# Optimization experiments

Measured on AMD Instinct MI355X. Metric: run time of the kernel, lower is better.

## Reference

```python
import jax, jax.numpy as jnp
import numpy as np

FEAT = 1433
HID = 2
NUM_CLASS = 7
EPS = 1e-5  # torch BatchNorm1d default eps


def _bn_softsign(h, gamma, beta):
    # BatchNorm1d in training mode: batch stats over (batch, length) per channel.
    mu = h.mean(axis=(0, 2), keepdims=True)
    var = h.var(axis=(0, 2), keepdims=True)  # biased, matches torch normalization
    hn = (h - mu) * jax.lax.rsqrt(var + EPS)
    hn = hn * gamma[None, :, None] + beta[None, :, None]
    return hn / (1.0 + jnp.abs(hn))  # Softsign


def feature_adjacency(x, y):
    # (x.unsqueeze(-1) * y.unsqueeze(-2)).sum(dim=1) with x channel dim == 1
    # reduces to an outer product of x[:,0] with neighbor.sum over K.
    adj = jnp.einsum('bf,bg->bfg', x.sum(1), y.sum(1))  # [B,F,F]
    adj = adj + jnp.swapaxes(adj, -1, -2)
    adj = jnp.sqrt(adj)
    # row_normalize: divide by sum over dim 1, zero out inf/nan
    norm = adj / adj.sum(axis=1, keepdims=True)
    norm = jnp.where(jnp.isfinite(norm), norm, 0.0)
    return norm + jnp.eye(FEAT, dtype=x.dtype)


def featbrd(x, adj, W, b):
    # adjacency-based feature conv: y[b,c,f] = sum_g adj[(b),f,g] x[b,c,g],
    # then 1x1 conv over channels (Conv1d kernel_size=1).
    if adj.shape[0] == 1:
        y = jnp.einsum('fg,bcg->bcf', adj[0], x)
    else:
        y = jnp.einsum('bfg,bcg->bcf', adj, x)
    return jnp.einsum('oc,bcf->bof', W, y) + b[None, :, None]


def setup_inputs() -> dict:
    key = jax.random.key(0)
    ks = jax.random.split(key, 10)
    B, K = 64, 8
    inp = {
        'x': jax.random.uniform(ks[0], (B, 1, FEAT), dtype=jnp.float32),
        'neighbor': jax.random.uniform(ks[1], (B, K, FEAT), dtype=jnp.float32),
        'adj_buf': jnp.zeros((1, FEAT, FEAT), jnp.float32),
        'W1': jax.random.normal(ks[2], (HID, 1), jnp.float32) * 0.5,
        'b1': jnp.zeros((HID,), jnp.float32),
        'W2': jax.random.normal(ks[3], (HID, HID), jnp.float32) * 0.5,
        'b2': jnp.zeros((HID,), jnp.float32),
        'g1': jnp.ones((HID,), jnp.float32),
        'be1': jnp.zeros((HID,), jnp.float32),
        'g2': jnp.ones((HID,), jnp.float32),
        'be2': jnp.zeros((HID,), jnp.float32),
        'Wc': jax.random.normal(ks[4], (NUM_CLASS, FEAT * HID), jnp.float32) * 0.02,
        'bc': jnp.zeros((NUM_CLASS,), jnp.float32),
    }
    return inp


def reference(x, neighbor, adj_buf, W1, b1, W2, b2, g1, be1, g2, be2, Wc, bc):
    fadj = feature_adjacency(x, neighbor)          # [B,F,F]
    adj_tot = adj_buf + fadj.sum(0)                # [1,F,F] (buffer starts at zero)
    h = _bn_softsign(featbrd(x, fadj, W1, b1), g1, be1)      # [B,HID,F]
    h = _bn_softsign(featbrd(h, adj_tot, W2, b2), g2, be2)   # [B,HID,F]
    flat = h.reshape(h.shape[0], -1)               # Flatten (C then F, row-major)
    return flat @ Wc.T + bc
```

## Files before the change

### kernel.cpp

```cpp
#include <hip/hip_runtime.h>
#include <hip/hip_bf16.h>
#include <math.h>

constexpr int F   = 1433;
constexpr int NB  = 64;
constexpr int KN  = 8;
constexpr int BF  = NB * F;
constexpr float EPS = 1e-5f;

constexpr int SF  = 16;
constexpr int CH  = 90;
constexpr int AbS = 1440;
constexpr int SK  = 15;
constexpr int FT  = 12;
constexpr int NA  = 720;
constexpr int NST = 256;

constexpr int O_YS  = 0;
constexpr int O_DP  = O_YS + BF;
constexpr int O_Y1P = O_DP + SF * BF;
constexpr int O_P   = O_Y1P + SF * BF;
constexpr int O_Y1  = O_P + 4 * BF;
constexpr int O_Y2  = O_Y1 + BF;
constexpr int O_G2P = O_Y2 + 2 * BF;
constexpr int O_AB  = O_G2P + SK * 128 * F;
constexpr int O_ST  = O_AB + (F * AbS) / 2;

__global__ __launch_bounds__(256) void k_D(const float* __restrict__ x,
                                           const float* __restrict__ nbr,
                                           float* __restrict__ DP,
                                           float* __restrict__ ys_out,
                                           float* __restrict__ st) {
  const int b = blockIdx.x, s = blockIdx.y;
  if (b == 0 && s == 0 && threadIdx.x < 64) st[threadIdx.x] = 0.f;
  __shared__ __align__(8) float2 xyc[CH];
  const int cs = s * CH, cn = min(CH, F - cs);
  for (int i = threadIdx.x; i < cn; i += 256) {
    const float* p = nbr + (size_t)b * KN * F + cs + i;
    float a = 0.f;
#pragma unroll
    for (int k = 0; k < KN; ++k) a += p[k * F];
    xyc[i] = make_float2(x[b * F + cs + i], a);
  }
  __syncthreads();
  float gx[6], gy[6], acc[6] = {};
#pragma unroll
  for (int j = 0; j < 6; ++j) {
    int g = threadIdx.x + 256 * j;
    int gc = min(g, F - 1);
    const float* p = nbr + (size_t)b * KN * F + gc;
    float a = 0.f;
#pragma unroll
    for (int k = 0; k < KN; ++k) a += p[k * F];
    gx[j] = (g < F) ? x[b * F + gc] : 0.f;
    gy[j] = (g < F) ? a : 0.f;
  }
  if (s == 0) {
#pragma unroll
    for (int j = 0; j < 6; ++j) {
      int g = threadIdx.x + 256 * j;
      if (g < F) ys_out[b * F + g] = gy[j];
    }
  }
#pragma unroll 6
  for (int i = 0; i < cn; ++i) {
    float2 p = xyc[i];
#pragma unroll
    for (int j = 0; j < 6; ++j)
      acc[j] += __builtin_amdgcn_sqrtf(fmaf(gy[j], p.x, gx[j] * p.y));
  }
#pragma unroll
  for (int j = 0; j < 6; ++j) {
    int g = threadIdx.x + 256 * j;
    if (g < F) DP[(size_t)s * BF + b * F + g] = acc[j];
  }
}

__global__ __launch_bounds__(256) void k_y1(const float* __restrict__ x,
                                            const float* __restrict__ ys,
                                            const float* __restrict__ DP,
                                            float* __restrict__ Y1P,
                                            float4* __restrict__ P) {
  __shared__ __align__(16) float4 pl[CH];
  const int b = blockIdx.x, s = blockIdx.y;
  const int cs = s * CH, cn = min(CH, F - cs);
  for (int i = threadIdx.x; i < cn; i += 256) {
    int g = cs + i;
    float d = 0.f;
#pragma unroll
    for (int t = 0; t < SF; ++t) d += DP[(size_t)t * BF + b * F + g];
    float inv = (d > 0.f) ? 1.f / d : 0.f;
    float xv = x[b * F + g], yv = ys[b * F + g];
    float4 pv = make_float4(xv, yv, xv * inv, inv);
    pl[i] = pv;
    P[b * F + g] = pv;
  }
  __syncthreads();
  float fx[6], fy[6], acc[6] = {};
#pragma unroll
  for (int j = 0; j < 6; ++j) {
    int f = threadIdx.x + 256 * j;
    fx[j] = (f < F) ? x[b * F + f] : 0.f;
    fy[j] = (f < F) ? ys[b * F + f] : 0.f;
  }
#pragma unroll 6
  for (int i = 0; i < cn; ++i) {
    float4 p = pl[i];
#pragma unroll
    for (int j = 0; j < 6; ++j)
      acc[j] = fmaf(__builtin_amdgcn_sqrtf(fmaf(fx[j], p.y, fy[j] * p.x)), p.z, acc[j]);
  }
#pragma unroll
  for (int j = 0; j < 6; ++j) {
    int f = threadIdx.x + 256 * j;
    if (f < F) Y1P[(size_t)s * BF + b * F + f] = acc[j];
  }
}

__global__ __launch_bounds__(256) void k_Astats(const float* __restrict__ x,
                                                const float* __restrict__ ys,
                                                const float4* __restrict__ P,
                                                const float* __restrict__ Y1P,
                                                __hip_bfloat16* __restrict__ Ab,
                                                float* __restrict__ y1,
                                                float* __restrict__ st) {
  const int bid = blockIdx.x;
  if (bid < NA) {
    __shared__ float2 fxy[FT][NB];
    const int gxc = bid % 6, fy = bid / 6;
    const int fbase = fy * FT;
#pragma unroll
    for (int r = 0; r < 3; ++r) {
      int i = threadIdx.x + 256 * r;
      int j = i >> 6, bb = i & 63;
      int f = fbase + j;
      float vx = 0.f, vy = 0.f;
      if (f < F) { vx = x[bb * F + f]; vy = ys[bb * F + f]; }
      fxy[j][bb] = make_float2(vx, vy);
    }
    __syncthreads();
    const int g = gxc * 256 + threadIdx.x;
    if (g >= AbS) return;
    if (g < F) {
      float acc[FT] = {};
      float4 cur[4], nxt[4];
#pragma unroll
      for (int t = 0; t < 4; ++t) cur[t] = P[t * F + g];
      for (int bb = 0; bb < NB; bb += 4) {
        if (bb + 4 < NB) {
#pragma unroll
          for (int t = 0; t < 4; ++t) nxt[t] = P[(bb + 4 + t) * F + g];
        }
#pragma unroll
        for (int t = 0; t < 4; ++t) {
          float4 pc = cur[t];
#pragma unroll
          for (int j = 0; j < FT; ++j) {
            float2 w = fxy[j][bb + t];
            acc[j] = fmaf(__builtin_amdgcn_sqrtf(fmaf(w.x, pc.y, pc.x * w.y)), pc.w, acc[j]);
          }
        }
#pragma unroll
        for (int t = 0; t < 4; ++t) cur[t] = nxt[t];
      }
#pragma unroll
      for (int j = 0; j < FT; ++j) {
        int f = fbase + j;
        if (f < F) Ab[(size_t)f * AbS + g] = __float2bfloat16(acc[j]);
      }
    } else {
#pragma unroll
      for (int j = 0; j < FT; ++j) {
        int f = fbase + j;
        if (f < F) Ab[(size_t)f * AbS + g] = __float2bfloat16(0.f);
      }
    }
  } else {
    const int sid = bid - NA;
    float sv = 0.f, sq = 0.f;
    for (int i = sid * 256 + threadIdx.x; i < BF; i += NST * 256) {
      float v = x[i];
#pragma unroll
      for (int t = 0; t < SF; ++t) v += Y1P[(size_t)t * BF + i];
      y1[i] = v;
      sv += v; sq += v * v;
    }
#pragma unroll
    for (int o = 32; o; o >>= 1) {
      sv += __shfl_down(sv, o, 64);
      sq += __shfl_down(sq, o, 64);
    }
    __shared__ float ls[4], lq[4];
    int wave = threadIdx.x >> 6, lane = threadIdx.x & 63;
    if (lane == 0) { ls[wave] = sv; lq[wave] = sq; }
    __syncthreads();
    if (threadIdx.x == 0) {
      atomicAdd(&st[0], ls[0] + ls[1] + ls[2] + ls[3]);
      atomicAdd(&st[1], lq[0] + lq[1] + lq[2] + lq[3]);
    }
  }
}

__global__ __launch_bounds__(256, 4) void k_gemm(const ushort* __restrict__ Ab,
                                                 const float* __restrict__ y1,
                                                 const float* __restrict__ st,
                                                 const float* __restrict__ W1,
                                                 const float* __restrict__ g1,
                                                 const float* __restrict__ be1,
                                                 float* __restrict__ G2P) {
  const float mu = st[0] / (float)BF;
  const float var = st[1] / (float)BF - mu * mu;
  const float wa = W1[0], wb = W1[1];
  const float k0 = wa * g1[0] / sqrtf(wa * wa * var + EPS);
  const float k1 = wb * g1[1] / sqrtf(wb * wb * var + EPS);
  const float c0 = -k0 * mu + be1[0];
  const float c1 = -k1 * mu + be1[1];

  __shared__ __align__(16) float Al[32 * 36];
  __shared__ __align__(16) float Hl[32 * 132];
  const int f0 = blockIdx.x * 32;
  const int gs = blockIdx.y * 96;
  const int tid = threadIdx.x;
  const int ffs = tid >> 3, g4s = (tid & 7) * 4;
  const int hb = tid & 7, hg = tid >> 3;
  const int fsub = (tid & 7) * 4, msub = (tid >> 3) * 4;

  uint2 pa; float pyv[8];
  auto loadRegs = [&](int gb) {
    const int f = f0 + ffs;
    pa = make_uint2(0u, 0u);
    if (f < F) pa = *(const uint2*)&Ab[(size_t)f * AbS + gb + g4s];
    const int gl = min(gb + hg, F - 1);
#pragma unroll
    for (int r = 0; r < 8; ++r) pyv[r] = y1[(hb + 8 * r) * F + gl];
  };
  auto storeLDS = [&]() {
    Al[(g4s + 0) * 36 + ffs] = __uint_as_float(pa.x << 16);
    Al[(g4s + 1) * 36 + ffs] = __uint_as_float(pa.x & 0xffff0000u);
    Al[(g4s + 2) * 36 + ffs] = __uint_as_float(pa.y << 16);
    Al[(g4s + 3) * 36 + ffs] = __uint_as_float(pa.y & 0xffff0000u);
#pragma unroll
    for (int r = 0; r < 8; ++r) {
      const int bb = hb + 8 * r;
      const float v = pyv[r];
      float h0 = fmaf(k0, v, c0); h0 = h0 / (1.f + fabsf(h0));
      float h1 = fmaf(k1, v, c1); h1 = h1 / (1.f + fabsf(h1));
      *(float2*)&Hl[hg * 132 + 2 * bb] = make_float2(h0, h1);
    }
  };

  float acc[4][4] = {};
  loadRegs(gs);
  for (int c = 0; c < 3; ++c) {
    if (c) __syncthreads();
    storeLDS();
    __syncthreads();
    if (c < 2) loadRegs(gs + (c + 1) * 32);
#pragma unroll 4
    for (int gi = 0; gi < 32; ++gi) {
      float4 a4 = *(const float4*)&Al[gi * 36 + fsub];
      float4 h4 = *(const float4*)&Hl[gi * 132 + msub];
      float av[4] = {a4.x, a4.y, a4.z, a4.w};
      float hv[4] = {h4.x, h4.y, h4.z, h4.w};
#pragma unroll
      for (int i = 0; i < 4; ++i)
#pragma unroll
        for (int j = 0; j < 4; ++j)
          acc[i][j] = fmaf(av[i], hv[j], acc[i][j]);
    }
  }
  float* dst = G2P + (size_t)blockIdx.y * 128 * F;
#pragma unroll
  for (int i = 0; i < 4; ++i) {
    int f = f0 + fsub + i;
    if (f < F) {
#pragma unroll
      for (int j = 0; j < 4; ++j)
        dst[(msub + j) * F + f] = acc[i][j];
    }
  }
}

__global__ __launch_bounds__(256) void k_stats2(const float* __restrict__ y1,
                                                const float* __restrict__ G2P,
                                                const float* __restrict__ st,
                                                const float* __restrict__ W1,
                                                const float* __restrict__ g1,
                                                const float* __restrict__ be1,
                                                float* __restrict__ y2,
                                                float* __restrict__ stw) {
  const float mu = st[0] / (float)BF;
  const float var = st[1] / (float)BF - mu * mu;
  const float wa = W1[0], wb = W1[1];
  const float k0 = wa * g1[0] / sqrtf(wa * wa * var + EPS);
  const float k1 = wb * g1[1] / sqrtf(wb * wb * var + EPS);
  const float c0 = -k0 * mu + be1[0];
  const float c1 = -k1 * mu + be1[1];

  float su = 0.f, sv = 0.f, suu = 0.f, svv = 0.f, suv = 0.f;
  for (int i = blockIdx.x * 256 + threadIdx.x; i < BF; i += gridDim.x * 256) {
    int b = i / F, f = i - b * F;
    float w = y1[i];
    float h0 = fmaf(k0, w, c0); h0 = h0 / (1.f + fabsf(h0));
    float h1 = fmaf(k1, w, c1); h1 = h1 / (1.f + fabsf(h1));
    int iu = (2 * b) * F + f, iv = iu + F;
    float u = 64.f * h0, v = 64.f * h1;
#pragma unroll
    for (int t = 0; t < SK; ++t) {
      u += G2P[(size_t)t * 128 * F + iu];
      v += G2P[(size_t)t * 128 * F + iv];
    }
    y2[iu] = u; y2[iv] = v;
    su += u; sv += v; suu += u * u; svv += v * v; suv += u * v;
  }
#pragma unroll
  for (int o = 32; o; o >>= 1) {
    su += __shfl_down(su, o, 64);
    sv += __shfl_down(sv, o, 64);
    suu += __shfl_down(suu, o, 64);
    svv += __shfl_down(svv, o, 64);
    suv += __shfl_down(suv, o, 64);
  }
  __shared__ float red[5][4];
  int wave = threadIdx.x >> 6, lane = threadIdx.x & 63;
  if (lane == 0) {
    red[0][wave] = su; red[1][wave] = sv; red[2][wave] = suu;
    red[3][wave] = svv; red[4][wave] = suv;
  }
  __syncthreads();
  if (threadIdx.x == 0) {
#pragma unroll
    for (int m = 0; m < 5; ++m)
      atomicAdd(&stw[2 + m], red[m][0] + red[m][1] + red[m][2] + red[m][3]);
  }
}

__global__ __launch_bounds__(256) void k_out(const float* __restrict__ y2,
                                             const float* __restrict__ st,
                                             const float* __restrict__ W2,
                                             const float* __restrict__ b2,
                                             const float* __restrict__ g2,
                                             const float* __restrict__ be2,
                                             const float* __restrict__ Wc,
                                             const float* __restrict__ bc,
                                             float* __restrict__ out) {
  float n = (float)BF;
  float Eu = st[2] / n, Ev = st[3] / n;
  float Euu = st[4] / n, Evv = st[5] / n, Euv = st[6] / n;
  float cA[2], cB[2], cC[2];
#pragma unroll
  for (int o = 0; o < 2; ++o) {
    float w0 = W2[o * 2 + 0], w1 = W2[o * 2 + 1];
    float mean = w0 * Eu + w1 * Ev + b2[o];
    float Eh2 = w0 * w0 * Euu + 2.f * w0 * w1 * Euv + w1 * w1 * Evv +
                2.f * b2[o] * (w0 * Eu + w1 * Ev) + b2[o] * b2[o];
    float vr = Eh2 - mean * mean;
    float inv = g2[o] / sqrtf(vr + EPS);
    cA[o] = w0 * inv;
    cB[o] = w1 * inv;
    cC[o] = (b2[o] - mean) * inv + be2[o];
  }
  const int b = blockIdx.x;
  float acc[7] = {};
  for (int f = threadIdx.x; f < F; f += 256) {
    float u = y2[(2 * b) * F + f], v = y2[(2 * b + 1) * F + f];
    float h0 = fmaf(cA[0], u, fmaf(cB[0], v, cC[0]));
    h0 = h0 / (1.f + fabsf(h0));
    float h1 = fmaf(cA[1], u, fmaf(cB[1], v, cC[1]));
    h1 = h1 / (1.f + fabsf(h1));
#pragma unroll
    for (int o = 0; o < 7; ++o) acc[o] = fmaf(Wc[o * (2 * F) + f], h0, acc[o]);
#pragma unroll
    for (int o = 0; o < 7; ++o) acc[o] = fmaf(Wc[o * (2 * F) + F + f], h1, acc[o]);
  }
#pragma unroll
  for (int o = 0; o < 7; ++o) {
#pragma unroll
    for (int s = 32; s; s >>= 1) acc[o] += __shfl_down(acc[o], s, 64);
  }
  __shared__ float red[7][4];
  int wave = threadIdx.x >> 6, lane = threadIdx.x & 63;
  if (lane == 0) {
#pragma unroll
    for (int o = 0; o < 7; ++o) red[o][wave] = acc[o];
  }
  __syncthreads();
  if (threadIdx.x < 7) {
    int o = threadIdx.x;
    out[b * 7 + o] = red[o][0] + red[o][1] + red[o][2] + red[o][3] + bc[o];
  }
}

extern "C" void kernel_launch(void* const* d_in, const int* in_sizes, int n_in,
                              void* d_out, int out_size, void* d_ws, size_t ws_size,
                              hipStream_t stream) {
  const float* x    = (const float*)d_in[0];
  const float* nbr  = (const float*)d_in[1];
  const float* W1   = (const float*)d_in[3];
  const float* W2   = (const float*)d_in[5];
  const float* b2   = (const float*)d_in[6];
  const float* g1   = (const float*)d_in[7];
  const float* be1  = (const float*)d_in[8];
  const float* g2   = (const float*)d_in[9];
  const float* be2  = (const float*)d_in[10];
  const float* Wc   = (const float*)d_in[11];
  const float* bc   = (const float*)d_in[12];
  float* out = (float*)d_out;
  float* ws  = (float*)d_ws;

  float*  ys  = ws + O_YS;
  float*  DP  = ws + O_DP;
  float*  Y1P = ws + O_Y1P;
  float4* P   = (float4*)(ws + O_P);
  float*  y1  = ws + O_Y1;
  float*  y2  = ws + O_Y2;
  float*  G2P = ws + O_G2P;
  __hip_bfloat16* Ab = (__hip_bfloat16*)(ws + O_AB);
  float*  st  = ws + O_ST;

  k_D     <<<dim3(NB, SF), 256, 0, stream>>>(x, nbr, DP, ys, st);
  k_y1    <<<dim3(NB, SF), 256, 0, stream>>>(x, ys, DP, Y1P, P);
  k_Astats<<<NA + NST, 256, 0, stream>>>(x, ys, P, Y1P, Ab, y1, st);
  k_gemm  <<<dim3(45, SK), 256, 0, stream>>>((const ushort*)Ab, y1, st, W1, g1, be1, G2P);
  k_stats2<<<NST, 256, 0, stream>>>(y1, G2P, st, W1, g1, be1, y2, st);
  k_out   <<<NB, 256, 0, stream>>>(y2, st, W2, b2, g2, be2, Wc, bc, out);
}
```

Measured before the change: 205.1 us.

## Fuse six-kernel pipeline into one persistent kernel with grid barriers

New measurement: 571.9 us. 2.79x slower.

```diff
diff --git a/kernel.cpp b/kernel.cpp
--- a/kernel.cpp
+++ b/kernel.cpp
@@ -25,6 +25,400 @@
 constexpr int O_G2P = O_Y2 + 2 * BF;
 constexpr int O_AB  = O_G2P + SK * 128 * F;
 constexpr int O_ST  = O_AB + (F * AbS) / 2;
+constexpr int O_BAR = O_ST + 64;
+
+__device__ __forceinline__ void grid_barrier(unsigned* cnt, unsigned* flag,
+                                             unsigned phase) {
+  __syncthreads();
+  if (threadIdx.x == 0) {
+    __threadfence();
+    unsigned t = atomicAdd(cnt, 1u);
+    if (t == phase * gridDim.x - 1u) {
+      __hip_atomic_store(flag, phase, __ATOMIC_RELEASE, __HIP_MEMORY_SCOPE_AGENT);
+    } else {
+      while (__hip_atomic_load(flag, __ATOMIC_ACQUIRE, __HIP_MEMORY_SCOPE_AGENT) < phase)
+        __builtin_amdgcn_s_sleep(2);
+    }
+    __threadfence();
+  }
+  __syncthreads();
+}
+
+__global__ __launch_bounds__(256, 4) void k_fused(
+    const float* __restrict__ x, const float* __restrict__ nbr,
+    const float* __restrict__ W1, const float* __restrict__ g1,
+    const float* __restrict__ be1, const float* __restrict__ W2,
+    const float* __restrict__ b2, const float* __restrict__ g2,
+    const float* __restrict__ be2, const float* __restrict__ Wc,
+    const float* __restrict__ bc, float* __restrict__ out,
+    float* __restrict__ ws) {
+  float*  ys  = ws + O_YS;
+  float*  DP  = ws + O_DP;
+  float*  Y1P = ws + O_Y1P;
+  float4* P   = (float4*)(ws + O_P);
+  float*  y1  = ws + O_Y1;
+  float*  y2  = ws + O_Y2;
+  float*  G2P = ws + O_G2P;
+  __hip_bfloat16* Ab = (__hip_bfloat16*)(ws + O_AB);
+  const ushort*   Abu = (const ushort*)(ws + O_AB);
+  float*  st  = ws + O_ST;
+  unsigned* bcnt  = (unsigned*)(ws + O_BAR);
+  unsigned* bflag = bcnt + 1;
+
+  __shared__ __align__(16) char smem[21504];
+  const int tid = threadIdx.x;
+  const int gsz = (int)gridDim.x;
+
+  {
+    float2* xyc = (float2*)smem;
+    for (int w = blockIdx.x; w < NB * SF; w += gsz) {
+      const int b = w & 63, s = w >> 6;
+      if (w == 0 && tid < 64) st[tid] = 0.f;
+      if (w == 1 && tid < NB * 7) out[tid] = bc[tid % 7];
+      __syncthreads();
+      const int cs = s * CH, cn = min(CH, F - cs);
+      for (int i = tid; i < cn; i += 256) {
+        const float* p = nbr + (size_t)b * KN * F + cs + i;
+        float a = 0.f;
+#pragma unroll
+        for (int k = 0; k < KN; ++k) a += p[k * F];
+        xyc[i] = make_float2(x[b * F + cs + i], a);
+      }
+      __syncthreads();
+      float gx[6], gy[6], acc[6] = {};
+#pragma unroll
+      for (int j = 0; j < 6; ++j) {
+        int g = tid + 256 * j;
+        int gc = min(g, F - 1);
+        const float* p = nbr + (size_t)b * KN * F + gc;
+        float a = 0.f;
+#pragma unroll
+        for (int k = 0; k < KN; ++k) a += p[k * F];
+        gx[j] = (g < F) ? x[b * F + gc] : 0.f;
+        gy[j] = (g < F) ? a : 0.f;
+      }
+      if (s == 0) {
+#pragma unroll
+        for (int j = 0; j < 6; ++j) {
+          int g = tid + 256 * j;
+          if (g < F) ys[b * F + g] = gy[j];
+        }
+      }
+#pragma unroll 6
+      for (int i = 0; i < cn; ++i) {
+        float2 p = xyc[i];
+#pragma unroll
+        for (int j = 0; j < 6; ++j)
+          acc[j] += __builtin_amdgcn_sqrtf(fmaf(gy[j], p.x, gx[j] * p.y));
+      }
+#pragma unroll
+      for (int j = 0; j < 6; ++j) {
+        int g = tid + 256 * j;
+        if (g < F) DP[(size_t)s * BF + b * F + g] = acc[j];
+      }
+    }
+  }
+  grid_barrier(bcnt, bflag, 1u);
+
+  {
+    float4* pl = (float4*)smem;
+    for (int w = blockIdx.x; w < NB * SF; w += gsz) {
+      const int b = w & 63, s = w >> 6;
+      __syncthreads();
+      const int cs = s * CH, cn = min(CH, F - cs);
+      for (int i = tid; i < cn; i += 256) {
+        int g = cs + i;
+        float d = 0.f;
+#pragma unroll
+        for (int t = 0; t < SF; ++t) d += DP[(size_t)t * BF + b * F + g];
+        float inv = (d > 0.f) ? 1.f / d : 0.f;
+        float xv = x[b * F + g], yv = ys[b * F + g];
+        float4 pv = make_float4(xv, yv, xv * inv, inv);
+        pl[i] = pv;
+        P[b * F + g] = pv;
+      }
+      __syncthreads();
+      float fx[6], fys[6], acc[6] = {};
+#pragma unroll
+      for (int j = 0; j < 6; ++j) {
+        int f = tid + 256 * j;
+        fx[j]  = (f < F) ? x[b * F + f] : 0.f;
+        fys[j] = (f < F) ? ys[b * F + f] : 0.f;
+      }
+#pragma unroll 6
+      for (int i = 0; i < cn; ++i) {
+        float4 p = pl[i];
+#pragma unroll
+        for (int j = 0; j < 6; ++j)
+          acc[j] = fmaf(__builtin_amdgcn_sqrtf(fmaf(fx[j], p.y, fys[j] * p.x)), p.z, acc[j]);
+      }
+#pragma unroll
+      for (int j = 0; j < 6; ++j) {
+        int f = tid + 256 * j;
+        if (f < F) Y1P[(size_t)s * BF + b * F + f] = acc[j];
+      }
+    }
+  }
+  grid_barrier(bcnt, bflag, 2u);
+
+  {
+    for (int w = blockIdx.x; w < NA + NST; w += gsz) {
+      __syncthreads();
+      if (w < NA) {
+        float2 (*fxy)[NB] = (float2(*)[NB])smem;
+        const int gxc = w % 6, fyt = w / 6;
+        const int fbase = fyt * FT;
+#pragma unroll
+        for (int r = 0; r < 3; ++r) {
+          int i = tid + 256 * r;
+          int j = i >> 6, bb = i & 63;
+          int f = fbase + j;
+          float vx = 0.f, vy = 0.f;
+          if (f < F) { vx = x[bb * F + f]; vy = ys[bb * F + f]; }
+          fxy[j][bb] = make_float2(vx, vy);
+        }
+        __syncthreads();
+        const int g = gxc * 256 + tid;
+        if (g < F) {
+          float acc[FT] = {};
+          float4 cur[4], nxt[4];
+#pragma unroll
+          for (int t = 0; t < 4; ++t) cur[t] = P[t * F + g];
+          for (int bb = 0; bb < NB; bb += 4) {
+            if (bb + 4 < NB) {
+#pragma unroll
+              for (int t = 0; t < 4; ++t) nxt[t] = P[(bb + 4 + t) * F + g];
+            }
+#pragma unroll
+            for (int t = 0; t < 4; ++t) {
+              float4 pc = cur[t];
+#pragma unroll
+              for (int j = 0; j < FT; ++j) {
+                float2 wv = fxy[j][bb + t];
+                acc[j] = fmaf(__builtin_amdgcn_sqrtf(fmaf(wv.x, pc.y, pc.x * wv.y)), pc.w, acc[j]);
+              }
+            }
+#pragma unroll
+            for (int t = 0; t < 4; ++t) cur[t] = nxt[t];
+          }
+#pragma unroll
+          for (int j = 0; j < FT; ++j) {
+            int f = fbase + j;
+            if (f < F) Ab[(size_t)f * AbS + g] = __float2bfloat16(acc[j]);
+          }
+        } else if (g < AbS) {
+#pragma unroll
+          for (int j = 0; j < FT; ++j) {
+            int f = fbase + j;
+            if (f < F) Ab[(size_t)f * AbS + g] = __float2bfloat16(0.f);
+          }
+        }
+      } else {
+        const int sid = w - NA;
+        float sv = 0.f, sq = 0.f;
+        for (int i = sid * 256 + tid; i < BF; i += NST * 256) {
+          float v = x[i];
+#pragma unroll
+          for (int t = 0; t < SF; ++t) v += Y1P[(size_t)t * BF + i];
+          y1[i] = v;
+          sv += v; sq += v * v;
+        }
+#pragma unroll
+        for (int o = 32; o; o >>= 1) {
+          sv += __shfl_down(sv, o, 64);
+          sq += __shfl_down(sq, o, 64);
+        }
+        float* ls = (float*)smem;
+        float* lq = ls + 4;
+        int wave = tid >> 6, lane = tid & 63;
+        if (lane == 0) { ls[wave] = sv; lq[wave] = sq; }
+        __syncthreads();
+        if (tid == 0) {
+          atomicAdd(&st[0], ls[0] + ls[1] + ls[2] + ls[3]);
+          atomicAdd(&st[1], lq[0] + lq[1] + lq[2] + lq[3]);
+        }
+      }
+    }
+  }
+  grid_barrier(bcnt, bflag, 3u);
+
+  {
+    const float mu  = st[0] / (float)BF;
+    const float var = st[1] / (float)BF - mu * mu;
+    const float wa = W1[0], wb = W1[1];
+    const float k0 = wa * g1[0] / sqrtf(wa * wa * var + EPS);
+    const float k1 = wb * g1[1] / sqrtf(wb * wb * var + EPS);
+    const float c0 = -k0 * mu + be1[0];
+    const float c1 = -k1 * mu + be1[1];
+
+    float* Al = (float*)smem;
+    float* Hl = (float*)(smem + 4608);
+    const int ffs = tid >> 3, g4s = (tid & 7) * 4;
+    const int hb = tid & 7, hg = tid >> 3;
+    const int fsub = (tid & 7) * 4, msub = (tid >> 3) * 4;
+
+    for (int w = blockIdx.x; w < 45 * SK; w += gsz) {
+      const int fb = w % 45, sk = w / 45;
+      const int f0 = fb * 32;
+      const int gs = sk * 96;
+      __syncthreads();
+
+      uint2 pa; float pyv[8];
+      auto loadRegs = [&](int gb) {
+        const int f = f0 + ffs;
+        pa = make_uint2(0u, 0u);
+        if (f < F) pa = *(const uint2*)&Abu[(size_t)f * AbS + gb + g4s];
+        const int gl = min(gb + hg, F - 1);
+#pragma unroll
+        for (int r = 0; r < 8; ++r) pyv[r] = y1[(hb + 8 * r) * F + gl];
+      };
+      auto storeLDS = [&]() {
+        Al[(g4s + 0) * 36 + ffs] = __uint_as_float(pa.x << 16);
+        Al[(g4s + 1) * 36 + ffs] = __uint_as_float(pa.x & 0xffff0000u);
+        Al[(g4s + 2) * 36 + ffs] = __uint_as_float(pa.y << 16);
+        Al[(g4s + 3) * 36 + ffs] = __uint_as_float(pa.y & 0xffff0000u);
+#pragma unroll
+        for (int r = 0; r < 8; ++r) {
+          const int bb = hb + 8 * r;
+          const float v = pyv[r];
+          float h0 = fmaf(k0, v, c0); h0 = h0 / (1.f + fabsf(h0));
+          float h1 = fmaf(k1, v, c1); h1 = h1 / (1.f + fabsf(h1));
+          *(float2*)&Hl[hg * 132 + 2 * bb] = make_float2(h0, h1);
+        }
+      };
+
+      float acc[4][4] = {};
+      loadRegs(gs);
+      for (int c = 0; c < 3; ++c) {
+        if (c) __syncthreads();
+        storeLDS();
+        __syncthreads();
+        if (c < 2) loadRegs(gs + (c + 1) * 32);
+#pragma unroll 4
+        for (int gi = 0; gi < 32; ++gi) {
+          float4 a4 = *(const float4*)&Al[gi * 36 + fsub];
+          float4 h4 = *(const float4*)&Hl[gi * 132 + msub];
+          float av[4] = {a4.x, a4.y, a4.z, a4.w};
+          float hv[4] = {h4.x, h4.y, h4.z, h4.w};
+#pragma unroll
+          for (int i = 0; i < 4; ++i)
+#pragma unroll
+            for (int j = 0; j < 4; ++j)
+              acc[i][j] = fmaf(av[i], hv[j], acc[i][j]);
+        }
+      }
+      float* dst = G2P + (size_t)sk * 128 * F;
+#pragma unroll
+      for (int i = 0; i < 4; ++i) {
+        int f = f0 + fsub + i;
+        if (f < F) {
+#pragma unroll
+          for (int j = 0; j < 4; ++j)
+            dst[(msub + j) * F + f] = acc[i][j];
+        }
+      }
+    }
+  }
+  grid_barrier(bcnt, bflag, 4u);
+
+  {
+    const float mu  = st[0] / (float)BF;
+    const float var = st[1] / (float)BF - mu * mu;
+    const float wa = W1[0], wb = W1[1];
+    const float k0 = wa * g1[0] / sqrtf(wa * wa * var + EPS);
+    const float k1 = wb * g1[1] / sqrtf(wb * wb * var + EPS);
+    const float c0 = -k0 * mu + be1[0];
+    const float c1 = -k1 * mu + be1[1];
+
+    float su = 0.f, sv = 0.f, suu = 0.f, svv = 0.f, suv = 0.f;
+    for (int i = blockIdx.x * 256 + tid; i < BF; i += gsz * 256) {
+      int b = i / F, f = i - b * F;
+      float wv = y1[i];
+      float h0 = fmaf(k0, wv, c0); h0 = h0 / (1.f + fabsf(h0));
+      float h1 = fmaf(k1, wv, c1); h1 = h1 / (1.f + fabsf(h1));
+      int iu = (2 * b) * F + f, iv = iu + F;
+      float u = 64.f * h0, v = 64.f * h1;
+#pragma unroll
+      for (int t = 0; t < SK; ++t) {
+        u += G2P[(size_t)t * 128 * F + iu];
+        v += G2P[(size_t)t * 128 * F + iv];
+      }
+      y2[iu] = u; y2[iv] = v;
+      su += u; sv += v; suu += u * u; svv += v * v; suv += u * v;
+    }
+#pragma unroll
+    for (int o = 32; o; o >>= 1) {
+      su  += __shfl_down(su, o, 64);
+      sv  += __shfl_down(sv, o, 64);
+      suu += __shfl_down(suu, o, 64);
+      svv += __shfl_down(svv, o, 64);
+      suv += __shfl_down(suv, o, 64);
+    }
+    float (*red)[4] = (float(*)[4])smem;
+    int wave = tid >> 6, lane = tid & 63;
+    if (lane == 0) {
+      red[0][wave] = su; red[1][wave] = sv; red[2][wave] = suu;
+      red[3][wave] = svv; red[4][wave] = suv;
+    }
+    __syncthreads();
+    if (tid == 0) {
+#pragma unroll
+      for (int m = 0; m < 5; ++m)
+        atomicAdd(&st[2 + m], red[m][0] + red[m][1] + red[m][2] + red[m][3]);
+    }
+  }
+  grid_barrier(bcnt, bflag, 5u);
+
+  {
+    float n = (float)BF;
+    float Eu = st[2] / n, Ev = st[3] / n;
+    float Euu = st[4] / n, Evv = st[5] / n, Euv = st[6] / n;
+    float cA[2], cB[2], cC[2];
+#pragma unroll
+    for (int o = 0; o < 2; ++o) {
+      float w0 = W2[o * 2 + 0], w1 = W2[o * 2 + 1];
+      float mean = w0 * Eu + w1 * Ev + b2[o];
+      float Eh2 = w0 * w0 * Euu + 2.f * w0 * w1 * Euv + w1 * w1 * Evv +
+                  2.f * b2[o] * (w0 * Eu + w1 * Ev) + b2[o] * b2[o];
+      float vr = Eh2 - mean * mean;
+      float inv = g2[o] / sqrtf(vr + EPS);
+      cA[o] = w0 * inv;
+      cB[o] = w1 * inv;
+      cC[o] = (b2[o] - mean) * inv + be2[o];
+    }
+    float (*red)[4] = (float(*)[4])smem;
+    for (int w = blockIdx.x; w < NB * 6; w += gsz) {
+      const int b = w / 6, part = w % 6;
+      float acc[7] = {};
+      const int f = part * 256 + tid;
+      if (f < F) {
+        float u = y2[(2 * b) * F + f], v = y2[(2 * b + 1) * F + f];
+        float h0 = fmaf(cA[0], u, fmaf(cB[0], v, cC[0]));
+        h0 = h0 / (1.f + fabsf(h0));
+        float h1 = fmaf(cA[1], u, fmaf(cB[1], v, cC[1]));
+        h1 = h1 / (1.f + fabsf(h1));
+#pragma unroll
+        for (int o = 0; o < 7; ++o)
+          acc[o] = fmaf(Wc[o * (2 * F) + f], h0, Wc[o * (2 * F) + F + f] * h1);
+      }
+#pragma unroll
+      for (int o = 0; o < 7; ++o) {
+#pragma unroll
+        for (int s2 = 32; s2; s2 >>= 1) acc[o] += __shfl_down(acc[o], s2, 64);
+      }
+      __syncthreads();
+      int wave = tid >> 6, lane = tid & 63;
+      if (lane == 0) {
+#pragma unroll
+        for (int o = 0; o < 7; ++o) red[o][wave] = acc[o];
+      }
+      __syncthreads();
+      if (tid < 7)
+        atomicAdd(&out[b * 7 + tid],
+                  red[tid][0] + red[tid][1] + red[tid][2] + red[tid][3]);
+    }
+  }
+}
 
 __global__ __launch_bounds__(256) void k_D(const float* __restrict__ x,
                                            const float* __restrict__ nbr,
@@ -418,10 +812,31 @@
   __hip_bfloat16* Ab = (__hip_bfloat16*)(ws + O_AB);
   float*  st  = ws + O_ST;
 
-  k_D     <<<dim3(NB, SF), 256, 0, stream>>>(x, nbr, DP, ys, st);
-  k_y1    <<<dim3(NB, SF), 256, 0, stream>>>(x, ys, DP, Y1P, P);
-  k_Astats<<<NA + NST, 256, 0, stream>>>(x, ys, P, Y1P, Ab, y1, st);
-  k_gemm  <<<dim3(45, SK), 256, 0, stream>>>((const ushort*)Ab, y1, st, W1, g1, be1, G2P);
-  k_stats2<<<NST, 256, 0, stream>>>(y1, G2P, st, W1, g1, be1, y2, st);
-  k_out   <<<NB, 256, 0, stream>>>(y2, st, W2, b2, g2, be2, Wc, bc, out);
+  static int nblk = -1;
+  if (nblk < 0) {
+    int dev = 0;
+    (void)hipGetDevice(&dev);
+    int cus = 0;
+    if (hipDeviceGetAttribute(&cus, hipDeviceAttributeMultiprocessorCount, dev) != hipSuccess || cus <= 0)
+      cus = 256;
+    int nb = 0;
+    if (hipOccupancyMaxActiveBlocksPerMultiprocessor(
+            &nb, reinterpret_cast<const void*>(&k_fused), 256, 0) != hipSuccess)
+      nb = 0;
+    long cap = (long)nb * (long)cus;
+    nblk = (cap >= 1024) ? 1024 : (int)cap;
+  }
+
+  if (nblk >= 256) {
+    hipMemsetAsync((void*)(ws + O_BAR), 0, 2 * sizeof(unsigned), stream);
+    k_fused<<<dim3(nblk), dim3(256), 0, stream>>>(x, nbr, W1, g1, be1, W2, b2,
+                                                  g2, be2, Wc, bc, out, ws);
+  } else {
+    k_D     <<<dim3(NB, SF), 256, 0, stream>>>(x, nbr, DP, ys, st);
+    k_y1    <<<dim3(NB, SF), 256, 0, stream>>>(x, ys, DP, Y1P, P);
+    k_Astats<<<NA + NST, 256, 0, stream>>>(x, ys, P, Y1P, Ab, y1, st);
+    k_gemm  <<<dim3(45, SK), 256, 0, stream>>>((const ushort*)Ab, y1, st, W1, g1, be1, G2P);
+    k_stats2<<<NST, 256, 0, stream>>>(y1, G2P, st, W1, g1, be1, y2, st);
+    k_out   <<<NB, 256, 0, stream>>>(y2, st, W2, b2, g2, be2, Wc, bc, out);
+  }
 }
```

## Compute neighbor sums once in separate kernel and deepen GEMM K-split

Applied to the files above, without the earlier changes.

Measured after the change: 205.9 us. No clear change (+0.4%).

```diff
diff --git a/kernel.cpp b/kernel.cpp
--- a/kernel.cpp
+++ b/kernel.cpp
@@ -11,7 +11,7 @@
 constexpr int SF  = 16;
 constexpr int CH  = 90;
 constexpr int AbS = 1440;
-constexpr int SK  = 15;
+constexpr int SK  = 9;
 constexpr int FT  = 12;
 constexpr int NA  = 720;
 constexpr int NST = 256;
@@ -26,41 +26,37 @@
 constexpr int O_AB  = O_G2P + SK * 128 * F;
 constexpr int O_ST  = O_AB + (F * AbS) / 2;
 
+__global__ __launch_bounds__(256) void k_ys(const float* __restrict__ nbr,
+                                            float* __restrict__ ys,
+                                            float* __restrict__ st) {
+  const int b = blockIdx.x, q = blockIdx.y;
+  if (b == 0 && q == 0 && threadIdx.x < 64) st[threadIdx.x] = 0.f;
+  const int g = q * 256 + threadIdx.x;
+  if (g < F) {
+    const float* p = nbr + (size_t)b * KN * F + g;
+    float a = 0.f;
+#pragma unroll
+    for (int k = 0; k < KN; ++k) a += p[k * F];
+    ys[b * F + g] = a;
+  }
+}
+
 __global__ __launch_bounds__(256) void k_D(const float* __restrict__ x,
-                                           const float* __restrict__ nbr,
-                                           float* __restrict__ DP,
-                                           float* __restrict__ ys_out,
-                                           float* __restrict__ st) {
+                                           const float* __restrict__ ys,
+                                           float* __restrict__ DP) {
   const int b = blockIdx.x, s = blockIdx.y;
-  if (b == 0 && s == 0 && threadIdx.x < 64) st[threadIdx.x] = 0.f;
   __shared__ __align__(8) float2 xyc[CH];
   const int cs = s * CH, cn = min(CH, F - cs);
-  for (int i = threadIdx.x; i < cn; i += 256) {
-    const float* p = nbr + (size_t)b * KN * F + cs + i;
-    float a = 0.f;
-#pragma unroll
-    for (int k = 0; k < KN; ++k) a += p[k * F];
-    xyc[i] = make_float2(x[b * F + cs + i], a);
-  }
+  for (int i = threadIdx.x; i < cn; i += 256)
+    xyc[i] = make_float2(x[b * F + cs + i], ys[b * F + cs + i]);
   __syncthreads();
   float gx[6], gy[6], acc[6] = {};
 #pragma unroll
   for (int j = 0; j < 6; ++j) {
     int g = threadIdx.x + 256 * j;
     int gc = min(g, F - 1);
-    const float* p = nbr + (size_t)b * KN * F + gc;
-    float a = 0.f;
-#pragma unroll
-    for (int k = 0; k < KN; ++k) a += p[k * F];
     gx[j] = (g < F) ? x[b * F + gc] : 0.f;
-    gy[j] = (g < F) ? a : 0.f;
-  }
-  if (s == 0) {
-#pragma unroll
-    for (int j = 0; j < 6; ++j) {
-      int g = threadIdx.x + 256 * j;
-      if (g < F) ys_out[b * F + g] = gy[j];
-    }
+    gy[j] = (g < F) ? ys[b * F + gc] : 0.f;
   }
 #pragma unroll 6
   for (int i = 0; i < cn; ++i) {
@@ -219,7 +215,7 @@
   __shared__ __align__(16) float Al[32 * 36];
   __shared__ __align__(16) float Hl[32 * 132];
   const int f0 = blockIdx.x * 32;
-  const int gs = blockIdx.y * 96;
+  const int gs = blockIdx.y * 160;
   const int tid = threadIdx.x;
   const int ffs = tid >> 3, g4s = (tid & 7) * 4;
   const int hb = tid & 7, hg = tid >> 3;
@@ -251,11 +247,11 @@
 
   float acc[4][4] = {};
   loadRegs(gs);
-  for (int c = 0; c < 3; ++c) {
+  for (int c = 0; c < 5; ++c) {
     if (c) __syncthreads();
     storeLDS();
     __syncthreads();
-    if (c < 2) loadRegs(gs + (c + 1) * 32);
+    if (c < 4) loadRegs(gs + (c + 1) * 32);
 #pragma unroll 4
     for (int gi = 0; gi < 32; ++gi) {
       float4 a4 = *(const float4*)&Al[gi * 36 + fsub];
@@ -418,7 +414,8 @@
   __hip_bfloat16* Ab = (__hip_bfloat16*)(ws + O_AB);
   float*  st  = ws + O_ST;
 
-  k_D     <<<dim3(NB, SF), 256, 0, stream>>>(x, nbr, DP, ys, st);
+  k_ys    <<<dim3(NB, 6), 256, 0, stream>>>(nbr, ys, st);
+  k_D     <<<dim3(NB, SF), 256, 0, stream>>>(x, ys, DP);
   k_y1    <<<dim3(NB, SF), 256, 0, stream>>>(x, ys, DP, Y1P, P);
   k_Astats<<<NA + NST, 256, 0, stream>>>(x, ys, P, Y1P, Ab, y1, st);
   k_gemm  <<<dim3(45, SK), 256, 0, stream>>>((const ushort*)Ab, y1, st, W1, g1, be1, G2P);
```
